# Kernel optimization log

Hardware: AMD Instinct MI355X
Metric: run time of the kernel (lower is better)

The kernel has to match this reference:

```python
import jax, jax.numpy as jnp
import numpy as np

HEADS = 8
GS = 16
C = 512
E = 512
SCALE = (E / HEADS) ** -0.5
PNAMES = ['sa_qkv_w','sa_qkv_b','sa_pa_w','sa_pa_b','sa_ln1_g','sa_ln1_b','sa_f1_w','sa_f1_b','sa_f2_w','sa_f2_b','sa_ln2_g','sa_ln2_b','sa_c1_w','sa_c1_b','sa_c2_w','sa_c2_b','sa_bn_g','sa_bn_b','ca_q_w','ca_q_b','ca_k_w','ca_k_b','ca_v_w','ca_v_b','ca_pa_w','ca_pa_b','p_q_w','p_q_b','p_k_w','p_k_b','p_v_w','p_v_b','p_pa_w','p_pa_b','p_ln_g','p_ln_b','p_lin_w','p_lin_b']


def _ln(x, g, b, eps=1e-5):
    m = x.mean(-1, keepdims=True)
    v = jnp.var(x, axis=-1, keepdims=True)
    return (x - m) / jnp.sqrt(v + eps) * g + b


def _conv1x1(x, w, b):
    return jnp.einsum('bchw,oc->bohw', x, w) + b[None, :, None, None]


def _up_ac(x, out=GS):
    # bilinear upsample, align_corners=True (nn.UpsamplingBilinear2d)
    H = x.shape[2]
    pos = jnp.arange(out) * (H - 1) / (out - 1)
    lo = jnp.floor(pos).astype(jnp.int32)
    hi = jnp.minimum(lo + 1, H - 1)
    w = (pos - lo).astype(x.dtype)
    xr = x[:, :, lo, :] * (1 - w)[None, None, :, None] + x[:, :, hi, :] * w[None, None, :, None]
    return xr[:, :, :, lo] * (1 - w) + xr[:, :, :, hi] * w


def _asri(x, p):
    # Sequence_ASRI: GAP tokens -> attention over the batch axis -> pixel-shuffle back
    B = x.shape[0]; ch = E // HEADS
    gap = x.mean((2, 3))                                             # [B,C]
    qkv = (gap @ p['sa_qkv_w'].T + p['sa_qkv_b']).reshape(B, 4, ch, HEADS).transpose(1, 3, 0, 2)  # [4,H,B,ch]
    q, k, v, skip = qkv[0], qkv[1], qkv[2], qkv[3]
    attn = jax.nn.softmax(jnp.einsum('hbc,hdc->hbd', q, k) * SCALE, -1)  # [H,B,B]
    o = jnp.einsum('hbd,hdc->hbc', attn, v)
    merge = lambda t: t.transpose(1, 2, 0).reshape(B, E)             # 'head b c -> b (c head)'
    a = merge(o) @ p['sa_pa_w'].T + p['sa_pa_b'] + merge(skip)
    h = jax.nn.relu(_ln(a, p['sa_ln1_g'], p['sa_ln1_b']) @ p['sa_f1_w'].T + p['sa_f1_b'])
    a = h @ p['sa_f2_w'].T + p['sa_f2_b'] + a
    s = _ln(a, p['sa_ln2_g'], p['sa_ln2_b']) @ p['sa_c1_w'].T + p['sa_c1_b']  # [B,C*16]
    s = _up_ac(s.reshape(B, C, 4, 4))                                 # pixel shuffle p1=p2=4 then bilinear to 16x16
    s = _conv1x1(s, p['sa_c2_w'], p['sa_c2_b'])
    # BatchNorm2d in eval mode (running_mean=0, running_var=1, eps=1e-5)
    s = s / np.float32(np.sqrt(1.0 + 1e-5)) * p['sa_bn_g'][None, :, None, None] + p['sa_bn_b'][None, :, None, None]
    return x + jax.nn.relu(s)


def _sscm(x1, x2, p):
    # Sequence_SSCM: GAP-token q/k over batch axis, full spatial v
    B = x1.shape[0]; ch = E // HEADS
    q = (x1.mean((2, 3)) @ p['ca_q_w'].T + p['ca_q_b']).reshape(B, ch, HEADS).transpose(2, 0, 1)  # [H,B,ch]
    k = (x2.mean((2, 3)) @ p['ca_k_w'].T + p['ca_k_b']).reshape(B, ch, HEADS).transpose(2, 0, 1)
    v = _conv1x1(x2, p['ca_v_w'], p['ca_v_b']).reshape(B, ch, HEADS, GS, GS).transpose(2, 0, 1, 3, 4).reshape(HEADS, B, ch * GS * GS)
    attn = jax.nn.softmax(jnp.einsum('hbc,hdc->hbd', q, k) * SCALE, -1)  # [H,B,B]
    o = jnp.einsum('hbd,hdm->hbm', attn, v)
    o = o.reshape(HEADS, B, ch, GS, GS).transpose(1, 2, 0, 3, 4).reshape(B, E, GS, GS)
    return jax.nn.relu(_conv1x1(o, p['ca_pa_w'], p['ca_pa_b']))


def _pixel(x1, x2, p):
    # Pixel_SSCM: pixel-wise cross-batch attention (no scale -- matches source)
    B = x1.shape[0]; ch = E // HEADS; N = GS * GS
    split = lambda t: t.reshape(B, ch, HEADS, N).transpose(2, 0, 3, 1)   # 'b (c head) h w -> head b (h w) c'
    q = split(_conv1x1(x1, p['p_q_w'], p['p_q_b']))                      # [H,B,N,ch]
    k = split(_conv1x1(x2, p['p_k_w'], p['p_k_b']))
    v = split(_conv1x1(x2, p['p_v_w'], p['p_v_b'])).reshape(HEADS, B * N, ch)
    attn = jax.nn.softmax(jnp.einsum('hbnc,hqmc->hbqnm', q, k), -1)      # [H,B,B,N,N]
    attn = attn.transpose(1, 0, 3, 2, 4).reshape(B, HEADS, N, B * N)     # 'head b q h w -> b head h (q w)'
    o = jnp.einsum('bhnm,hmc->bhnc', attn, v)
    o = o.transpose(0, 3, 1, 2).reshape(B, E, GS, GS)                    # 'b head (h w) c -> b (c head) h w'
    o = _conv1x1(o, p['p_pa_w'], p['p_pa_b']) + x1
    t = o.reshape(B, C, N).transpose(0, 2, 1)                            # [B,N,C]
    t = jax.nn.relu(_ln(t, p['p_ln_g'], p['p_ln_b']) @ p['p_lin_w'].T + p['p_lin_b'])
    return t.transpose(0, 2, 1).reshape(B, C, GS, GS)


def _hrlm(p, xs, xq):
    sa_s = _asri(xs, p)
    sa_q = _asri(xq, p)
    ca_s = _sscm(sa_s, sa_q, p)
    ca_q = _sscm(sa_q, sa_s, p)
    return _pixel(sa_s, ca_q, p), _pixel(sa_q, ca_s, p)


def setup_inputs():
    key = jax.random.key(0)
    ks = iter(jax.random.split(key, 64))
    w = lambda *s: (jax.random.normal(next(ks), s) * 0.02).astype(jnp.float32)
    z = lambda n: jnp.zeros((n,), jnp.float32)
    o = lambda n: jnp.ones((n,), jnp.float32)
    return dict(
        fea_support=jax.random.normal(next(ks), (8, C, GS, GS), jnp.float32),
        fea_query=jax.random.normal(next(ks), (8, C, GS, GS), jnp.float32),
        sa_qkv_w=w(4 * E, C), sa_qkv_b=z(4 * E),
        sa_pa_w=w(E, E), sa_pa_b=z(E),
        sa_ln1_g=o(E), sa_ln1_b=z(E),
        sa_f1_w=w(E, E), sa_f1_b=z(E), sa_f2_w=w(E, E), sa_f2_b=z(E),
        sa_ln2_g=o(E), sa_ln2_b=z(E),
        sa_c1_w=w(C * 16, E), sa_c1_b=z(C * 16),
        sa_c2_w=w(C, E), sa_c2_b=z(C),
        sa_bn_g=o(C), sa_bn_b=z(C),
        ca_q_w=w(E, C), ca_q_b=z(E), ca_k_w=w(E, C), ca_k_b=z(E),
        ca_v_w=w(E, C), ca_v_b=z(E), ca_pa_w=w(C, E), ca_pa_b=z(C),
        p_q_w=w(E, C), p_q_b=z(E), p_k_w=w(E, C), p_k_b=z(E),
        p_v_w=w(E, C), p_v_b=z(E), p_pa_w=w(C, E), p_pa_b=z(C),
        p_ln_g=o(C), p_ln_b=z(C), p_lin_w=w(C, C), p_lin_b=z(C),
    )


def reference(fea_support, fea_query, sa_qkv_w, sa_qkv_b, sa_pa_w, sa_pa_b, sa_ln1_g, sa_ln1_b, sa_f1_w, sa_f1_b, sa_f2_w, sa_f2_b, sa_ln2_g, sa_ln2_b, sa_c1_w, sa_c1_b, sa_c2_w, sa_c2_b, sa_bn_g, sa_bn_b, ca_q_w, ca_q_b, ca_k_w, ca_k_b, ca_v_w, ca_v_b, ca_pa_w, ca_pa_b, p_q_w, p_q_b, p_k_w, p_k_b, p_v_w, p_v_b, p_pa_w, p_pa_b, p_ln_g, p_ln_b, p_lin_w, p_lin_b):
    p = dict(zip(PNAMES, (sa_qkv_w, sa_qkv_b, sa_pa_w, sa_pa_b, sa_ln1_g, sa_ln1_b, sa_f1_w, sa_f1_b, sa_f2_w, sa_f2_b, sa_ln2_g, sa_ln2_b, sa_c1_w, sa_c1_b, sa_c2_w, sa_c2_b, sa_bn_g, sa_bn_b, ca_q_w, ca_q_b, ca_k_w, ca_k_b, ca_v_w, ca_v_b, ca_pa_w, ca_pa_b, p_q_w, p_q_b, p_k_w, p_k_b, p_v_w, p_v_b, p_pa_w, p_pa_b, p_ln_g, p_ln_b, p_lin_w, p_lin_b)))
    return _hrlm(p, fea_support, fea_query)
```

## Files before the change

### kernel.cpp

```cpp
#include <hip/hip_runtime.h>
#include <cmath>

#define IMG 131072
#define BIGF 1048576

#define CF_RELU  1
#define CF_RES   2
#define CF_BN    4
#define CF_SPLIT 8
#define CF_TRANS 16

typedef __attribute__((ext_vector_type(8))) short short8;
typedef __attribute__((ext_vector_type(4))) short short4v;
typedef __attribute__((ext_vector_type(4))) float f32x4;

__device__ __forceinline__ float wave_sum(float v){
    #pragma unroll
    for (int off = 32; off; off >>= 1) v += __shfl_xor(v, off);
    return v;
}

__device__ __forceinline__ unsigned short bf16_rn(float x){
    union { float f; unsigned u; } v; v.f = x;
    unsigned r = v.u + 0x7FFF + ((v.u >> 16) & 1);
    return (unsigned short)(r >> 16);
}
__device__ __forceinline__ float bf16_to_f(unsigned short h){
    union { float f; unsigned u; } v; v.u = ((unsigned)h) << 16;
    return v.f;
}
__device__ __forceinline__ unsigned pk_hi(unsigned a, unsigned b){
    return __builtin_amdgcn_perm(b, a, 0x05040100u);
}
__device__ __forceinline__ unsigned pk_lo(unsigned a, unsigned b){
    return __builtin_amdgcn_perm(b, a, 0x07060302u);
}

struct GapJobs  { const float* x[2]; float* o[2]; };
struct G8Job    { const float* in; const float* W; const float* bias; const float* add; float* out; };
struct G8Jobs   { G8Job j[4]; };
struct AAJobs   { const float* qkv[2]; float* om[2]; };
struct LnJobs   { const float* in[2]; float* out[2]; };
struct UpJobs   { const float* in[2]; float* out[2]; };
struct SAJobs   { const float* q8[2]; const float* k8[2]; float* aw[2]; };
struct SPJobs   { const float* aw[2]; const float* v[2]; float* out[2]; };
struct ZJobs    { float* p[2]; };
struct ConvJob  { const float* X; const float* W; const float* B; const float* R;
                  const float* bng; const float* bnb; float* O; int flags; };
struct ConvJobs { ConvJob j[6]; };
struct PixJob   { const unsigned* Q; const unsigned* K; const unsigned* V; float* O; };
struct PixJobs  { PixJob j[2]; };

__global__ __launch_bounds__(64) void k_gap(GapJobs jo){
    const int br = blockIdx.y;
    const int bc = blockIdx.x;
    const int lane = threadIdx.x;
    const float* p = jo.x[br] + (size_t)bc * 256;
    float s = p[lane] + p[lane + 64] + p[lane + 128] + p[lane + 192];
    s = wave_sum(s);
    if (lane == 0) jo.o[br][bc] = s * (1.0f / 256.0f);
}

__global__ __launch_bounds__(64) void k_gemm8(G8Jobs jo, int add_off, int add_stride, int O, int relu){
    const G8Job j = jo.j[blockIdx.y];
    const int o = blockIdx.x;
    const int lane = threadIdx.x;
    const float* wr = j.W + (size_t)o * 512;
    float acc[8] = {0,0,0,0,0,0,0,0};
    #pragma unroll
    for (int i = 0; i < 8; i++){
        float w = wr[lane + 64*i];
        #pragma unroll
        for (int b = 0; b < 8; b++) acc[b] += w * j.in[b*512 + lane + 64*i];
    }
    #pragma unroll
    for (int b = 0; b < 8; b++) acc[b] = wave_sum(acc[b]);
    if (lane < 8){
        float v = acc[0];
        #pragma unroll
        for (int b = 1; b < 8; b++) if (lane == b) v = acc[b];
        v += j.bias[o];
        if (j.add) v += j.add[lane*add_stride + add_off + o];
        if (relu) v = fmaxf(v, 0.f);
        j.out[(size_t)lane * O + o] = v;
    }
}

__global__ __launch_bounds__(64) void k_asri_attn(AAJobs jo){
    const int br = blockIdx.y;
    const float* qkv = jo.qkv[br];
    const int h = blockIdx.x >> 3, b = blockIdx.x & 7, c = threadIdx.x;
    const int ci = c*8 + h;
    float qc = qkv[b*2048 + ci];
    float s[8];
    #pragma unroll
    for (int d = 0; d < 8; d++){
        float p = qc * qkv[d*2048 + 512 + ci];
        p = wave_sum(p);
        s[d] = p * 0.125f;
    }
    float m = s[0];
    #pragma unroll
    for (int d = 1; d < 8; d++) m = fmaxf(m, s[d]);
    float sum = 0.f;
    #pragma unroll
    for (int d = 0; d < 8; d++){ s[d] = __expf(s[d]-m); sum += s[d]; }
    float r = 1.f / sum;
    float oc = 0.f;
    #pragma unroll
    for (int d = 0; d < 8; d++) oc += s[d]*r * qkv[d*2048 + 1024 + ci];
    jo.om[br][b*512 + ci] = oc;
}

__global__ __launch_bounds__(64) void k_ln8(LnJobs jo,
    const float* __restrict__ g, const float* __restrict__ be)
{
    const int br = blockIdx.y;
    const int b = blockIdx.x, lane = threadIdx.x;
    const float* in = jo.in[br];
    float v[8]; float s = 0.f;
    #pragma unroll
    for (int i = 0; i < 8; i++){ v[i] = in[b*512 + lane + 64*i]; s += v[i]; }
    s = wave_sum(s);
    float mean = s * (1.f/512.f);
    float q = 0.f;
    #pragma unroll
    for (int i = 0; i < 8; i++){ float d = v[i]-mean; q += d*d; }
    q = wave_sum(q);
    float rstd = rsqrtf(q*(1.f/512.f) + 1e-5f);
    #pragma unroll
    for (int i = 0; i < 8; i++){
        int c = lane + 64*i;
        jo.out[br][b*512 + c] = (v[i]-mean)*rstd*g[c] + be[c];
    }
}

__global__ __launch_bounds__(256) void k_up(UpJobs jo){
    const int br = blockIdx.y;
    const int idx = blockIdx.x*256 + threadIdx.x;
    const int x = idx & 15, y = (idx >> 4) & 15, bc = idx >> 8;
    float px = (float)(x*3) / 15.0f, py = (float)(y*3) / 15.0f;
    int lx = (int)px, ly = (int)py;
    float wx = px - lx, wy = py - ly;
    int hx = min(lx+1, 3), hy = min(ly+1, 3);
    const float* p = jo.in[br] + (size_t)bc * 16;
    float v00 = p[ly*4+lx], v01 = p[ly*4+hx], v10 = p[hy*4+lx], v11 = p[hy*4+hx];
    float a0 = v00*(1.f-wy) + v10*wy;
    float a1 = v01*(1.f-wy) + v11*wy;
    jo.out[br][idx] = a0*(1.f-wx) + a1*wx;
}

__global__ __launch_bounds__(256) void k_zero(ZJobs jo){
    jo.p[blockIdx.y][(size_t)blockIdx.x*256 + threadIdx.x] = 0.f;
}

#define LDK 40
__device__ __forceinline__ void convm_body(
    const float* __restrict__ Xb, const float* __restrict__ W,
    const float* __restrict__ bias, const float* __restrict__ resb,
    const float* __restrict__ bng, const float* __restrict__ bnb, float bninv,
    float* __restrict__ outb, int flags, int o0, int n0, unsigned short* lds)
{
    const int tid512 = threadIdx.x;
    const int g   = tid512 >> 8;
    const int tid = tid512 & 255;
    unsigned short* sAh = lds + g*10240;
    unsigned short* sAl = sAh + 2560;
    unsigned short* sBh = sAl + 2560;
    unsigned short* sBl = sBh + 2560;
    const int wv = tid >> 6, lane = tid & 63;
    const int quad = lane >> 4, l16 = lane & 15;
    const int wo = (wv >> 1) * 32, wn = (wv & 1) * 32;
    const int so  = tid >> 2, sk8 = (tid & 3) * 8;
    const int sp  = tid & 15, sn  = (tid >> 4) * 4;

    const bool trans = (flags & CF_TRANS) != 0;
    int so_g = o0 + so;
    if (trans) so_g = ((so_g & 63) << 3) | (so_g >> 6);

    const float* wrow = W + (size_t)so_g*512 + g*256 + sk8;
    const float* xrow = Xb + (size_t)(g*256 + 2*sp)*256 + n0 + sn;

    f32x4 acc[2][2] = {};
    float4 a0 = *(const float4*)(wrow);
    float4 a1 = *(const float4*)(wrow + 4);
    float4 x0 = *(const float4*)(xrow);
    float4 x1 = *(const float4*)(xrow + 256);

    for (int k0 = 0; k0 < 256; k0 += 32){
        __syncthreads();
        {
            float wa[8] = {a0.x,a0.y,a0.z,a0.w,a1.x,a1.y,a1.z,a1.w};
            #pragma unroll
            for (int j = 0; j < 4; j++){
                unsigned short h0 = bf16_rn(wa[2*j]);
                unsigned short h1 = bf16_rn(wa[2*j+1]);
                unsigned short g0 = bf16_rn(wa[2*j]   - bf16_to_f(h0));
                unsigned short g1 = bf16_rn(wa[2*j+1] - bf16_to_f(h1));
                *(unsigned*)&sAh[so*LDK + sk8 + 2*j] = (unsigned)h0 | ((unsigned)h1 << 16);
                *(unsigned*)&sAl[so*LDK + sk8 + 2*j] = (unsigned)g0 | ((unsigned)g1 << 16);
            }
            float xe[4] = {x0.x,x0.y,x0.z,x0.w};
            float xo[4] = {x1.x,x1.y,x1.z,x1.w};
            #pragma unroll
            for (int j = 0; j < 4; j++){
                unsigned short h0 = bf16_rn(xe[j]);
                unsigned short h1 = bf16_rn(xo[j]);
                unsigned short g0 = bf16_rn(xe[j] - bf16_to_f(h0));
                unsigned short g1 = bf16_rn(xo[j] - bf16_to_f(h1));
                *(unsigned*)&sBh[(sn+j)*LDK + 2*sp] = (unsigned)h0 | ((unsigned)h1 << 16);
                *(unsigned*)&sBl[(sn+j)*LDK + 2*sp] = (unsigned)g0 | ((unsigned)g1 << 16);
            }
        }
        __syncthreads();
        if (k0 + 32 < 256){
            a0 = *(const float4*)(wrow + k0 + 32);
            a1 = *(const float4*)(wrow + k0 + 36);
            x0 = *(const float4*)(xrow + (size_t)(k0+32)*256);
            x1 = *(const float4*)(xrow + (size_t)(k0+32)*256 + 256);
        }
        short8 ah[2], al[2], bh[2], bl[2];
        #pragma unroll
        for (int t = 0; t < 2; t++){
            int ai = (wo + 16*t + l16)*LDK + quad*8;
            ah[t] = *(const short8*)&sAh[ai];
            al[t] = *(const short8*)&sAl[ai];
            int bi = (wn + 16*t + l16)*LDK + quad*8;
            bh[t] = *(const short8*)&sBh[bi];
            bl[t] = *(const short8*)&sBl[bi];
        }
        if (trans){
            #pragma unroll
            for (int mt = 0; mt < 2; mt++){
                #pragma unroll
                for (int nt = 0; nt < 2; nt++){
                    acc[mt][nt] = __builtin_amdgcn_mfma_f32_16x16x32_bf16(bh[nt], ah[mt], acc[mt][nt], 0, 0, 0);
                    acc[mt][nt] = __builtin_amdgcn_mfma_f32_16x16x32_bf16(bl[nt], ah[mt], acc[mt][nt], 0, 0, 0);
                    acc[mt][nt] = __builtin_amdgcn_mfma_f32_16x16x32_bf16(bh[nt], al[mt], acc[mt][nt], 0, 0, 0);
                }
            }
        } else {
            #pragma unroll
            for (int mt = 0; mt < 2; mt++){
                #pragma unroll
                for (int nt = 0; nt < 2; nt++){
                    acc[mt][nt] = __builtin_amdgcn_mfma_f32_16x16x32_bf16(ah[mt], bh[nt], acc[mt][nt], 0, 0, 0);
                    acc[mt][nt] = __builtin_amdgcn_mfma_f32_16x16x32_bf16(ah[mt], bl[nt], acc[mt][nt], 0, 0, 0);
                    acc[mt][nt] = __builtin_amdgcn_mfma_f32_16x16x32_bf16(al[mt], bh[nt], acc[mt][nt], 0, 0, 0);
                }
            }
        }
    }
    __syncthreads();
    float* red = (float*)lds;
    if (g == 1){
        float* r = red + tid*20;
        #pragma unroll
        for (int mt = 0; mt < 2; mt++)
            #pragma unroll
            for (int nt = 0; nt < 2; nt++)
                *(f32x4*)(r + (mt*2+nt)*4) = acc[mt][nt];
    }
    __syncthreads();
    if (g == 0){
        float* r = red + tid*20;
        #pragma unroll
        for (int mt = 0; mt < 2; mt++)
            #pragma unroll
            for (int nt = 0; nt < 2; nt++){
                f32x4 o4 = *(const f32x4*)(r + (mt*2+nt)*4);
                acc[mt][nt] += o4;
            }
        if (trans){
            unsigned* op = (unsigned*)outb;
            #pragma unroll
            for (int mt = 0; mt < 2; mt++){
                #pragma unroll
                for (int nt = 0; nt < 2; nt++){
                    const int p  = o0 + wo + 16*mt + l16;
                    const int nb = n0 + wn + 16*nt + quad*4;
                    const int osrc = ((p & 63) << 3) | (p >> 6);
                    const float bs = bias[osrc];
                    #pragma unroll
                    for (int rr = 0; rr < 4; rr++){
                        float v = acc[mt][nt][rr] + bs;
                        unsigned short hi = bf16_rn(v);
                        unsigned short lo = bf16_rn(v - bf16_to_f(hi));
                        op[(size_t)(nb+rr)*512 + p] = (unsigned)hi | ((unsigned)lo << 16);
                    }
                }
            }
        } else {
            #pragma unroll
            for (int mt = 0; mt < 2; mt++){
                #pragma unroll
                for (int nt = 0; nt < 2; nt++){
                    const int n  = n0 + wn + 16*nt + l16;
                    const int ob = o0 + wo + 16*mt + quad*4;
                    #pragma unroll
                    for (int rr = 0; rr < 4; rr++){
                        const int o = ob + rr;
                        float v = acc[mt][nt][rr] + bias[o];
                        if (flags & CF_BN)   v = v*(bninv*bng[o]) + bnb[o];
                        if (flags & CF_RELU) v = fmaxf(v, 0.f);
                        if (flags & CF_RES)  v += resb[(size_t)o*256 + n];
                        if (flags & CF_SPLIT){
                            unsigned short hi = bf16_rn(v);
                            unsigned short lo = bf16_rn(v - bf16_to_f(hi));
                            unsigned pk = (unsigned)hi | ((unsigned)lo << 16);
                            ((unsigned*)outb)[(size_t)o*256 + n] = pk;
                        } else {
                            outb[(size_t)o*256 + n] = v;
                        }
                    }
                }
            }
        }
    }
}

__global__ __launch_bounds__(512) void k_convm(ConvJobs jo, float bninv)
{
    __shared__ unsigned short lds[20480];
    const int z = blockIdx.z;
    const ConvJob j = jo.j[z >> 3];
    const int b = z & 7;
    convm_body(j.X + (size_t)b*IMG, j.W, j.B, j.R ? j.R + (size_t)b*IMG : nullptr,
               j.bng, j.bnb, bninv, j.O + (size_t)b*IMG, j.flags,
               blockIdx.y*64, blockIdx.x*64, lds);
}

__global__ __launch_bounds__(64) void k_sscm_attn(SAJobs jo)
{
    const int br = blockIdx.y;
    const int h = blockIdx.x >> 3, b = blockIdx.x & 7, c = threadIdx.x;
    const int ci = c*8 + h;
    float qc = jo.q8[br][b*512 + ci];
    float s[8];
    #pragma unroll
    for (int d = 0; d < 8; d++){
        float p = qc * jo.k8[br][d*512 + ci];
        p = wave_sum(p);
        s[d] = p * 0.125f;
    }
    float m = s[0];
    #pragma unroll
    for (int d = 1; d < 8; d++) m = fmaxf(m, s[d]);
    float sum = 0.f;
    #pragma unroll
    for (int d = 0; d < 8; d++){ s[d] = __expf(s[d]-m); sum += s[d]; }
    float r = 1.f/sum;
    if (c < 8){
        float v = s[0];
        #pragma unroll
        for (int d = 1; d < 8; d++) if (c == d) v = s[d];
        jo.aw[br][blockIdx.x*8 + c] = v*r;
    }
}

__global__ __launch_bounds__(256) void k_sscm_apply(SPJobs jo)
{
    const int br = blockIdx.y;
    const int idx = blockIdx.x*256 + threadIdx.x;
    const int pix = idx & 255, e = (idx >> 8) & 511, b = idx >> 17;
    const int h = e & 7;
    const float* aw = jo.aw[br] + (h*8 + b)*8;
    const float* v = jo.v[br];
    float acc = 0.f;
    #pragma unroll
    for (int d = 0; d < 8; d++) acc += aw[d] * v[(size_t)d*IMG + (size_t)e*256 + pix];
    jo.out[br][idx] = acc;
}

__global__ __launch_bounds__(256) void k_pixel_mfma(PixJobs jo)
{
    __shared__ char smem[40960];
    unsigned short* sQh = (unsigned short*)smem;
    unsigned short* sQl = sQh + 2*64*40;
    unsigned short* sKh = sQl + 2*64*40;
    unsigned short* sKl = sKh + 2*64*40;
    unsigned short* sP  = (unsigned short*)smem;
    unsigned short* sVh = sKh;
    unsigned short* sVl = sKl;

    const int br = blockIdx.y >> 3, b = blockIdx.y & 7;
    const PixJob J = jo.j[br];
    const int nt = blockIdx.x & 3, d = blockIdx.x >> 2;
    const int h = blockIdx.z;
    const int tid = threadIdx.x;
    const int wv = tid >> 6, lane = tid & 63;
    const int quad = lane >> 4, l16 = lane & 15;
    const int n0 = nt * 64;

    {
        const unsigned* Qt = J.Q + (size_t)b*IMG + (size_t)n0*512 + h*64;
        const int q = tid >> 2, i0 = (tid & 3) * 16;
        const unsigned* src = Qt + (size_t)q*512 + i0;
        uint4 w0 = *(const uint4*)(src);
        uint4 w1 = *(const uint4*)(src + 4);
        uint4 w2 = *(const uint4*)(src + 8);
        uint4 w3 = *(const uint4*)(src + 12);
        unsigned hb[8], lb[8];
        hb[0]=pk_hi(w0.x,w0.y); hb[1]=pk_hi(w0.z,w0.w); hb[2]=pk_hi(w1.x,w1.y); hb[3]=pk_hi(w1.z,w1.w);
        hb[4]=pk_hi(w2.x,w2.y); hb[5]=pk_hi(w2.z,w2.w); hb[6]=pk_hi(w3.x,w3.y); hb[7]=pk_hi(w3.z,w3.w);
        lb[0]=pk_lo(w0.x,w0.y); lb[1]=pk_lo(w0.z,w0.w); lb[2]=pk_lo(w1.x,w1.y); lb[3]=pk_lo(w1.z,w1.w);
        lb[4]=pk_lo(w2.x,w2.y); lb[5]=pk_lo(w2.z,w2.w); lb[6]=pk_lo(w3.x,w3.y); lb[7]=pk_lo(w3.z,w3.w);
        int dst = (i0>>5)*2560 + q*40 + (i0&31);
        *(uint4*)&sQh[dst]     = *(uint4*)&hb[0];
        *(uint4*)&sQh[dst + 8] = *(uint4*)&hb[4];
        *(uint4*)&sQl[dst]     = *(uint4*)&lb[0];
        *(uint4*)&sQl[dst + 8] = *(uint4*)&lb[4];
    }
    __syncthreads();

    short8 bqh[2], bql[2];
    #pragma unroll
    for (int ks = 0; ks < 2; ks++){
        int idx = ks*2560 + (wv*16 + l16)*40 + quad*8;
        bqh[ks] = *(const short8*)&sQh[idx];
        bql[ks] = *(const short8*)&sQl[idx];
    }

    f32x4 S[16] = {};
    #pragma unroll
    for (int mq = 0; mq < 4; mq++){
        if (mq) __syncthreads();
        {
            const unsigned* Kt = J.K + (size_t)d*IMG + (size_t)(mq*64)*512 + h*64;
            const int mloc = tid & 63, cb0 = tid >> 6;
            #pragma unroll
            for (int p = 0; p < 2; p++){
                int cb = cb0 + 4*p;
                const unsigned* src = Kt + (size_t)mloc*512 + cb*8;
                uint4 wa = *(const uint4*)(src);
                uint4 wb = *(const uint4*)(src + 4);
                union { short8 s; unsigned u[4]; } hu, lu;
                hu.u[0]=pk_hi(wa.x,wa.y); hu.u[1]=pk_hi(wa.z,wa.w);
                hu.u[2]=pk_hi(wb.x,wb.y); hu.u[3]=pk_hi(wb.z,wb.w);
                lu.u[0]=pk_lo(wa.x,wa.y); lu.u[1]=pk_lo(wa.z,wa.w);
                lu.u[2]=pk_lo(wb.x,wb.y); lu.u[3]=pk_lo(wb.z,wb.w);
                int idx = (cb>>2)*2560 + mloc*40 + (cb&3)*8;
                *(short8*)&sKh[idx] = hu.s;
                *(short8*)&sKl[idx] = lu.s;
            }
        }
        __syncthreads();
        #pragma unroll
        for (int mtl = 0; mtl < 4; mtl++){
            int t = mq*4 + mtl;
            #pragma unroll
            for (int ks = 0; ks < 2; ks++){
                int idx = ks*2560 + (mtl*16 + l16)*40 + quad*8;
                short8 ah = *(const short8*)&sKh[idx];
                short8 al = *(const short8*)&sKl[idx];
                S[t] = __builtin_amdgcn_mfma_f32_16x16x32_bf16(ah, bqh[ks], S[t], 0, 0, 0);
                S[t] = __builtin_amdgcn_mfma_f32_16x16x32_bf16(ah, bql[ks], S[t], 0, 0, 0);
                S[t] = __builtin_amdgcn_mfma_f32_16x16x32_bf16(al, bqh[ks], S[t], 0, 0, 0);
            }
        }
    }

    {
        float mx = -3.4e38f;
        #pragma unroll
        for (int t = 0; t < 16; t++)
            #pragma unroll
            for (int r = 0; r < 4; r++) mx = fmaxf(mx, S[t][r]);
        mx = fmaxf(mx, __shfl_xor(mx, 16));
        mx = fmaxf(mx, __shfl_xor(mx, 32));
        float sum = 0.f;
        #pragma unroll
        for (int t = 0; t < 16; t++)
            #pragma unroll
            for (int r = 0; r < 4; r++){ S[t][r] = __expf(S[t][r]-mx); sum += S[t][r]; }
        sum += __shfl_xor(sum, 16);
        sum += __shfl_xor(sum, 32);
        float rr = 1.f/sum;
        #pragma unroll
        for (int t = 0; t < 16; t++)
            #pragma unroll
            for (int r = 0; r < 4; r++) S[t][r] *= rr;
    }

    f32x4 oac[4] = {};
    #pragma unroll
    for (int hm = 0; hm < 2; hm++){
        __syncthreads();
        #pragma unroll
        for (int mtl = 0; mtl < 8; mtl++){
            int t = hm*8 + mtl;
            short4v p4;
            #pragma unroll
            for (int r = 0; r < 4; r++) p4[r] = (short)bf16_rn(S[t][r]);
            int idx = (mtl>>1)*2560 + (wv*16 + l16)*40 + 16*(mtl&1) + quad*4;
            *(short4v*)&sP[idx] = p4;
        }
        #pragma unroll
        for (int sub = 0; sub < 2; sub++){
            if (sub) __syncthreads();
            {
                const unsigned* Vp = J.V + (size_t)d*IMG + (size_t)h*256 + hm*128 + sub*64;
                const int mp = tid & 31, c0 = tid >> 5;
                #pragma unroll
                for (int p = 0; p < 8; p++){
                    int c = c0 + 8*p;
                    const unsigned* src = Vp + (size_t)c*2048 + 2*mp;
                    uint2 w = *(const uint2*)(src);
                    int idx = ((2*mp)>>5)*2560 + c*40 + ((2*mp)&31);
                    *(unsigned*)&sVh[idx] = pk_hi(w.x, w.y);
                    *(unsigned*)&sVl[idx] = pk_lo(w.x, w.y);
                }
            }
            __syncthreads();
            #pragma unroll
            for (int l = 0; l < 2; l++){
                int gks = sub*2 + l;
                int pidx = gks*2560 + (wv*16 + l16)*40 + quad*8;
                short8 bp = *(const short8*)&sP[pidx];
                #pragma unroll
                for (int ct = 0; ct < 4; ct++){
                    int vidx = l*2560 + (ct*16 + l16)*40 + quad*8;
                    short8 vh = *(const short8*)&sVh[vidx];
                    short8 vl = *(const short8*)&sVl[vidx];
                    oac[ct] = __builtin_amdgcn_mfma_f32_16x16x32_bf16(vh, bp, oac[ct], 0, 0, 0);
                    oac[ct] = __builtin_amdgcn_mfma_f32_16x16x32_bf16(vl, bp, oac[ct], 0, 0, 0);
                }
            }
        }
    }

    {
        float* Ob = J.O + (size_t)b * IMG;
        const int q = n0 + wv*16 + l16;
        #pragma unroll
        for (int ct = 0; ct < 4; ct++){
            #pragma unroll
            for (int r = 0; r < 4; r++){
                int c = ct*16 + quad*4 + r;
                unsafeAtomicAdd(&Ob[(size_t)(c*8+h)*256 + q], oac[ct][r]);
            }
        }
    }
}

__global__ __launch_bounds__(64) void k_ln_pix(LnJobs jo,
    const float* __restrict__ g, const float* __restrict__ be)
{
    const int br = blockIdx.y;
    const int bn = blockIdx.x;
    const int b = bn >> 8, n = bn & 255;
    const int lane = threadIdx.x;
    const float* p = jo.in[br] + (size_t)b*IMG + n;
    float v[8]; float s = 0.f;
    #pragma unroll
    for (int i = 0; i < 8; i++){ v[i] = p[(size_t)(lane + 64*i)*256]; s += v[i]; }
    s = wave_sum(s);
    float mean = s * (1.f/512.f);
    float q = 0.f;
    #pragma unroll
    for (int i = 0; i < 8; i++){ float d = v[i]-mean; q += d*d; }
    q = wave_sum(q);
    float rstd = rsqrtf(q*(1.f/512.f) + 1e-5f);
    #pragma unroll
    for (int i = 0; i < 8; i++){
        int c = lane + 64*i;
        jo.out[br][(size_t)b*IMG + (size_t)c*256 + n] = (v[i]-mean)*rstd*g[c] + be[c];
    }
}

extern "C" void kernel_launch(void* const* d_in, const int* in_sizes, int n_in,
                              void* d_out, int out_size, void* d_ws, size_t ws_size,
                              hipStream_t stream)
{
    const float* xs    = (const float*)d_in[0];
    const float* xq    = (const float*)d_in[1];
    const float* qkvw  = (const float*)d_in[2];  const float* qkvb = (const float*)d_in[3];
    const float* paw   = (const float*)d_in[4];  const float* pab  = (const float*)d_in[5];
    const float* ln1g  = (const float*)d_in[6];  const float* ln1b = (const float*)d_in[7];
    const float* f1w   = (const float*)d_in[8];  const float* f1b  = (const float*)d_in[9];
    const float* f2w   = (const float*)d_in[10]; const float* f2b  = (const float*)d_in[11];
    const float* ln2g  = (const float*)d_in[12]; const float* ln2b = (const float*)d_in[13];
    const float* c1w   = (const float*)d_in[14]; const float* c1b  = (const float*)d_in[15];
    const float* c2w   = (const float*)d_in[16]; const float* c2b  = (const float*)d_in[17];
    const float* bng   = (const float*)d_in[18]; const float* bnb  = (const float*)d_in[19];
    const float* caqw  = (const float*)d_in[20]; const float* caqb = (const float*)d_in[21];
    const float* cakw  = (const float*)d_in[22]; const float* cakb = (const float*)d_in[23];
    const float* cavw  = (const float*)d_in[24]; const float* cavb = (const float*)d_in[25];
    const float* capw  = (const float*)d_in[26]; const float* capb = (const float*)d_in[27];
    const float* pqw   = (const float*)d_in[28]; const float* pqb  = (const float*)d_in[29];
    const float* pkw   = (const float*)d_in[30]; const float* pkb  = (const float*)d_in[31];
    const float* pvw   = (const float*)d_in[32]; const float* pvb  = (const float*)d_in[33];
    const float* ppw   = (const float*)d_in[34]; const float* ppb  = (const float*)d_in[35];
    const float* plng  = (const float*)d_in[36]; const float* plnb = (const float*)d_in[37];
    const float* plinw = (const float*)d_in[38]; const float* plinb= (const float*)d_in[39];

    const size_t SMF = 262144;
    float* ws = (float*)d_ws;
    float* smb = ws;
    float* B[12];
    for (int i = 0; i < 12; i++) B[i] = ws + SMF + (size_t)i*BIGF;
    float* sa_s = B[0]; float* sa_q = B[1];
    float* ca_s = B[2]; float* ca_q = B[3];
    const bool paired_pixel = ws_size >= (SMF + 12*(size_t)BIGF)*sizeof(float) + 1024;

    auto SM = [&](int br){ return smb + (size_t)br*131072; };
    auto GAP=[&](int br){ return SM(br); };            auto QKV=[&](int br){ return SM(br)+4096; };
    auto OM =[&](int br){ return SM(br)+20480; };      auto AA =[&](int br){ return SM(br)+24576; };
    auto HB =[&](int br){ return SM(br)+28672; };      auto A2 =[&](int br){ return SM(br)+32768; };
    auto LNB=[&](int br){ return SM(br)+36864; };      auto S8 =[&](int br){ return SM(br)+40960; };
    auto ATW=[&](int br){ return SM(br)+106496; };     auto Q8 =[&](int br){ return SM(br)+107008; };
    auto K8 =[&](int br){ return SM(br)+111104; };

    const float bninv = 1.0f / sqrtf(1.0f + 1e-5f);
    float* out0 = (float*)d_out;
    float* out1 = out0 + (size_t)BIGF;

    {
        GapJobs gj = {{xs, xq}, {GAP(0), GAP(1)}};
        k_gap<<<dim3(4096,2), 64, 0, stream>>>(gj);
        G8Jobs qj = {{{GAP(0), qkvw, qkvb, nullptr, QKV(0)}, {GAP(1), qkvw, qkvb, nullptr, QKV(1)}}};
        k_gemm8<<<dim3(2048,2), 64, 0, stream>>>(qj, 0, 0, 2048, 0);
        AAJobs aj = {{QKV(0), QKV(1)}, {OM(0), OM(1)}};
        k_asri_attn<<<dim3(64,2), 64, 0, stream>>>(aj);
        G8Jobs pj = {{{OM(0), paw, pab, QKV(0), AA(0)}, {OM(1), paw, pab, QKV(1), AA(1)}}};
        k_gemm8<<<dim3(512,2), 64, 0, stream>>>(pj, 1536, 2048, 512, 0);
        LnJobs l1 = {{AA(0), AA(1)}, {LNB(0), LNB(1)}};
        k_ln8<<<dim3(8,2), 64, 0, stream>>>(l1, ln1g, ln1b);
        G8Jobs fj = {{{LNB(0), f1w, f1b, nullptr, HB(0)}, {LNB(1), f1w, f1b, nullptr, HB(1)}}};
        k_gemm8<<<dim3(512,2), 64, 0, stream>>>(fj, 0, 0, 512, 1);
        G8Jobs f2j = {{{HB(0), f2w, f2b, AA(0), A2(0)}, {HB(1), f2w, f2b, AA(1), A2(1)}}};
        k_gemm8<<<dim3(512,2), 64, 0, stream>>>(f2j, 0, 512, 512, 0);
        LnJobs l2 = {{A2(0), A2(1)}, {LNB(0), LNB(1)}};
        k_ln8<<<dim3(8,2), 64, 0, stream>>>(l2, ln2g, ln2b);
        G8Jobs cj = {{{LNB(0), c1w, c1b, nullptr, S8(0)}, {LNB(1), c1w, c1b, nullptr, S8(1)}}};
        k_gemm8<<<dim3(8192,2), 64, 0, stream>>>(cj, 0, 0, 8192, 0);
        UpJobs uj = {{S8(0), S8(1)}, {B[4], B[5]}};
        k_up<<<dim3(4096,2), 256, 0, stream>>>(uj);
        ConvJobs c2j = {};
        c2j.j[0] = {B[4], c2w, c2b, xs, bng, bnb, sa_s, CF_BN|CF_RELU|CF_RES};
        c2j.j[1] = {B[5], c2w, c2b, xq, bng, bnb, sa_q, CF_BN|CF_RELU|CF_RES};
        k_convm<<<dim3(4,8,16), 512, 0, stream>>>(c2j, bninv);
    }

    {
        GapJobs gj = {{sa_s, sa_q}, {GAP(0), GAP(1)}};
        k_gap<<<dim3(4096,2), 64, 0, stream>>>(gj);
        G8Jobs qj = {{{GAP(0), caqw, caqb, nullptr, Q8(0)},
                      {GAP(1), cakw, cakb, nullptr, K8(0)},
                      {GAP(1), caqw, caqb, nullptr, Q8(1)},
                      {GAP(0), cakw, cakb, nullptr, K8(1)}}};
        k_gemm8<<<dim3(512,4), 64, 0, stream>>>(qj, 0, 0, 512, 0);
        SAJobs sj = {{Q8(0), Q8(1)}, {K8(0), K8(1)}, {ATW(0), ATW(1)}};
        k_sscm_attn<<<dim3(64,2), 64, 0, stream>>>(sj);
        ConvJobs vj = {};
        vj.j[0] = {sa_q, cavw, cavb, nullptr, nullptr, nullptr, B[4], 0};
        vj.j[1] = {sa_s, cavw, cavb, nullptr, nullptr, nullptr, B[5], 0};
        k_convm<<<dim3(4,8,16), 512, 0, stream>>>(vj, 1.f);
        SPJobs pj = {{ATW(0), ATW(1)}, {B[4], B[5]}, {B[6], B[7]}};
        k_sscm_apply<<<dim3(4096,2), 256, 0, stream>>>(pj);
        ConvJobs aj = {};
        aj.j[0] = {B[6], capw, capb, nullptr, nullptr, nullptr, ca_s, CF_RELU};
        aj.j[1] = {B[7], capw, capb, nullptr, nullptr, nullptr, ca_q, CF_RELU};
        k_convm<<<dim3(4,8,16), 512, 0, stream>>>(aj, 1.f);
    }

    if (paired_pixel){
        ConvJobs qkvj = {};
        qkvj.j[0] = {sa_s, pqw, pqb, nullptr, nullptr, nullptr, B[4],  CF_SPLIT|CF_TRANS};
        qkvj.j[1] = {ca_q, pkw, pkb, nullptr, nullptr, nullptr, B[5],  CF_SPLIT|CF_TRANS};
        qkvj.j[2] = {ca_q, pvw, pvb, nullptr, nullptr, nullptr, B[6],  CF_SPLIT};
        qkvj.j[3] = {sa_q, pqw, pqb, nullptr, nullptr, nullptr, B[8],  CF_SPLIT|CF_TRANS};
        qkvj.j[4] = {ca_s, pkw, pkb, nullptr, nullptr, nullptr, B[9],  CF_SPLIT|CF_TRANS};
        qkvj.j[5] = {ca_s, pvw, pvb, nullptr, nullptr, nullptr, B[10], CF_SPLIT};
        k_convm<<<dim3(4,8,48), 512, 0, stream>>>(qkvj, 1.f);
        ZJobs zj = {{B[7], B[11]}};
        k_zero<<<dim3(4096,2), 256, 0, stream>>>(zj);
        PixJobs pxj = {{{(const unsigned*)B[4], (const unsigned*)B[5], (const unsigned*)B[6], B[7]},
                        {(const unsigned*)B[8], (const unsigned*)B[9], (const unsigned*)B[10], B[11]}}};
        k_pixel_mfma<<<dim3(32,16,8), 256, 0, stream>>>(pxj);
        ConvJobs ppj = {};
        ppj.j[0] = {B[7],  ppw, ppb, sa_s, nullptr, nullptr, out0, CF_RES};
        ppj.j[1] = {B[11], ppw, ppb, sa_q, nullptr, nullptr, out1, CF_RES};
        k_convm<<<dim3(4,8,16), 512, 0, stream>>>(ppj, 1.f);
        LnJobs lj = {{out0, out1}, {B[4], B[8]}};
        k_ln_pix<<<dim3(2048,2), 64, 0, stream>>>(lj, plng, plnb);
        ConvJobs lnj = {};
        lnj.j[0] = {B[4], plinw, plinb, nullptr, nullptr, nullptr, out0, CF_RELU};
        lnj.j[1] = {B[8], plinw, plinb, nullptr, nullptr, nullptr, out1, CF_RELU};
        k_convm<<<dim3(4,8,16), 512, 0, stream>>>(lnj, 1.f);
    } else {
        auto pixel1 = [&](const float* x1, const float* x2, float* out){
            ConvJobs qkvj = {};
            qkvj.j[0] = {x1, pqw, pqb, nullptr, nullptr, nullptr, B[4], CF_SPLIT|CF_TRANS};
            qkvj.j[1] = {x2, pkw, pkb, nullptr, nullptr, nullptr, B[5], CF_SPLIT|CF_TRANS};
            qkvj.j[2] = {x2, pvw, pvb, nullptr, nullptr, nullptr, B[6], CF_SPLIT};
            k_convm<<<dim3(4,8,24), 512, 0, stream>>>(qkvj, 1.f);
            ZJobs zj = {{B[7], B[7]}};
            k_zero<<<dim3(4096,1), 256, 0, stream>>>(zj);
            PixJobs pxj = {{{(const unsigned*)B[4], (const unsigned*)B[5], (const unsigned*)B[6], B[7]},
                            {(const unsigned*)B[4], (const unsigned*)B[5], (const unsigned*)B[6], B[7]}}};
            k_pixel_mfma<<<dim3(32,8,8), 256, 0, stream>>>(pxj);
            ConvJobs ppj = {};
            ppj.j[0] = {B[7], ppw, ppb, x1, nullptr, nullptr, out, CF_RES};
            k_convm<<<dim3(4,8,8), 512, 0, stream>>>(ppj, 1.f);
            LnJobs lj = {{out, out}, {B[4], B[4]}};
            k_ln_pix<<<dim3(2048,1), 64, 0, stream>>>(lj, plng, plnb);
            ConvJobs lnj = {};
            lnj.j[0] = {B[4], plinw, plinb, nullptr, nullptr, nullptr, out, CF_RELU};
            k_convm<<<dim3(4,8,8), 512, 0, stream>>>(lnj, 1.f);
        };
        pixel1(sa_s, ca_q, out0);
        pixel1(sa_q, ca_s, out1);
    }

    (void)in_sizes; (void)n_in; (void)out_size;
}
```

Baseline: 473.6 us.

## Pre-split weights and activations into packed bf16 hi/lo once for reuse

A new kernel converts the eight conv weight matrices into packed bf16 hi/lo pairs once per call. Selected conv outputs also write a packed split copy that later convs load directly, so they skip the per-tile bf16 split arithmetic in the LDS staging loop. This removes repeated conversion ALU work across the many blocks that reuse the same weights and activations. In exchange it adds an extra weight pass, extra output writes, and workspace use. The new paths are gated on workspace size.

```diff
diff --git a/kernel.cpp b/kernel.cpp
--- a/kernel.cpp
+++ b/kernel.cpp
@@ -28,6 +28,11 @@
 __device__ __forceinline__ float bf16_to_f(unsigned short h){
     union { float f; unsigned u; } v; v.u = ((unsigned)h) << 16;
     return v.f;
+}
+__device__ __forceinline__ unsigned pack_split(float x){
+    unsigned short hi = bf16_rn(x);
+    unsigned short lo = bf16_rn(x - bf16_to_f(hi));
+    return (unsigned)hi | ((unsigned)lo << 16);
 }
 __device__ __forceinline__ unsigned pk_hi(unsigned a, unsigned b){
     return __builtin_amdgcn_perm(b, a, 0x05040100u);
@@ -45,8 +50,10 @@
 struct SAJobs   { const float* q8[2]; const float* k8[2]; float* aw[2]; };
 struct SPJobs   { const float* aw[2]; const float* v[2]; float* out[2]; };
 struct ZJobs    { float* p[2]; };
+struct WsJobs   { const float* w[8]; unsigned* o; };
 struct ConvJob  { const float* X; const float* W; const float* B; const float* R;
-                  const float* bng; const float* bnb; float* O; int flags; };
+                  const float* bng; const float* bnb; float* O; int flags;
+                  const unsigned* Wpk; const unsigned* Xpk; unsigned* O2; };
 struct ConvJobs { ConvJob j[6]; };
 struct PixJob   { const unsigned* Q; const unsigned* K; const unsigned* V; float* O; };
 struct PixJobs  { PixJob j[2]; };
@@ -154,12 +161,24 @@
     jo.p[blockIdx.y][(size_t)blockIdx.x*256 + threadIdx.x] = 0.f;
 }
 
+__global__ __launch_bounds__(256) void k_wsplit(WsJobs jo){
+    const int m = blockIdx.y;
+    const int i = (blockIdx.x*256 + threadIdx.x)*4;
+    float4 v = *(const float4*)(jo.w[m] + i);
+    uint4 r;
+    r.x = pack_split(v.x); r.y = pack_split(v.y);
+    r.z = pack_split(v.z); r.w = pack_split(v.w);
+    *(uint4*)(jo.o + (size_t)m*262144 + i) = r;
+}
+
 #define LDK 40
 __device__ __forceinline__ void convm_body(
-    const float* __restrict__ Xb, const float* __restrict__ W,
+    const float* __restrict__ Xb, const unsigned* __restrict__ Xpk,
+    const float* __restrict__ W,  const unsigned* __restrict__ Wpk,
     const float* __restrict__ bias, const float* __restrict__ resb,
     const float* __restrict__ bng, const float* __restrict__ bnb, float bninv,
-    float* __restrict__ outb, int flags, int o0, int n0, unsigned short* lds)
+    float* __restrict__ outb, unsigned* __restrict__ o2b,
+    int flags, int o0, int n0, unsigned short* lds)
 {
     const int tid512 = threadIdx.x;
     const int g   = tid512 >> 8;
@@ -178,18 +197,30 @@
     int so_g = o0 + so;
     if (trans) so_g = ((so_g & 63) << 3) | (so_g >> 6);
 
-    const float* wrow = W + (size_t)so_g*512 + g*256 + sk8;
-    const float* xrow = Xb + (size_t)(g*256 + 2*sp)*256 + n0 + sn;
+    const float*    wrow  = W + (size_t)so_g*512 + g*256 + sk8;
+    const unsigned* wprow = Wpk ? Wpk + (size_t)so_g*512 + g*256 + sk8 : nullptr;
+    const float*    xrow  = Xb + (size_t)(g*256 + 2*sp)*256 + n0 + sn;
+    const unsigned* xprow = Xpk ? Xpk + (size_t)(g*256 + 2*sp)*256 + n0 + sn : nullptr;
 
     f32x4 acc[2][2] = {};
-    float4 a0 = *(const float4*)(wrow);
-    float4 a1 = *(const float4*)(wrow + 4);
-    float4 x0 = *(const float4*)(xrow);
-    float4 x1 = *(const float4*)(xrow + 256);
+    float4 a0, a1, x0, x1;
+    uint4 pw0, pw1, px0, px1;
+    if (Wpk){ pw0 = *(const uint4*)(wprow); pw1 = *(const uint4*)(wprow + 4); }
+    else    { a0  = *(const float4*)(wrow); a1  = *(const float4*)(wrow + 4); }
+    if (Xpk){ px0 = *(const uint4*)(xprow); px1 = *(const uint4*)(xprow + 256); }
+    else    { x0  = *(const float4*)(xrow); x1  = *(const float4*)(xrow + 256); }
 
     for (int k0 = 0; k0 < 256; k0 += 32){
         __syncthreads();
-        {
+        if (Wpk){
+            uint4 h4, l4;
+            h4.x = pk_hi(pw0.x, pw0.y); h4.y = pk_hi(pw0.z, pw0.w);
+            h4.z = pk_hi(pw1.x, pw1.y); h4.w = pk_hi(pw1.z, pw1.w);
+            l4.x = pk_lo(pw0.x, pw0.y); l4.y = pk_lo(pw0.z, pw0.w);
+            l4.z = pk_lo(pw1.x, pw1.y); l4.w = pk_lo(pw1.z, pw1.w);
+            *(uint4*)&sAh[so*LDK + sk8] = h4;
+            *(uint4*)&sAl[so*LDK + sk8] = l4;
+        } else {
             float wa[8] = {a0.x,a0.y,a0.z,a0.w,a1.x,a1.y,a1.z,a1.w};
             #pragma unroll
             for (int j = 0; j < 4; j++){
@@ -200,6 +231,17 @@
                 *(unsigned*)&sAh[so*LDK + sk8 + 2*j] = (unsigned)h0 | ((unsigned)h1 << 16);
                 *(unsigned*)&sAl[so*LDK + sk8 + 2*j] = (unsigned)g0 | ((unsigned)g1 << 16);
             }
+        }
+        if (Xpk){
+            *(unsigned*)&sBh[(sn+0)*LDK + 2*sp] = pk_hi(px0.x, px1.x);
+            *(unsigned*)&sBl[(sn+0)*LDK + 2*sp] = pk_lo(px0.x, px1.x);
+            *(unsigned*)&sBh[(sn+1)*LDK + 2*sp] = pk_hi(px0.y, px1.y);
+            *(unsigned*)&sBl[(sn+1)*LDK + 2*sp] = pk_lo(px0.y, px1.y);
+            *(unsigned*)&sBh[(sn+2)*LDK + 2*sp] = pk_hi(px0.z, px1.z);
+            *(unsigned*)&sBl[(sn+2)*LDK + 2*sp] = pk_lo(px0.z, px1.z);
+            *(unsigned*)&sBh[(sn+3)*LDK + 2*sp] = pk_hi(px0.w, px1.w);
+            *(unsigned*)&sBl[(sn+3)*LDK + 2*sp] = pk_lo(px0.w, px1.w);
+        } else {
             float xe[4] = {x0.x,x0.y,x0.z,x0.w};
             float xo[4] = {x1.x,x1.y,x1.z,x1.w};
             #pragma unroll
@@ -214,10 +256,10 @@
         }
         __syncthreads();
         if (k0 + 32 < 256){
-            a0 = *(const float4*)(wrow + k0 + 32);
-            a1 = *(const float4*)(wrow + k0 + 36);
-            x0 = *(const float4*)(xrow + (size_t)(k0+32)*256);
-            x1 = *(const float4*)(xrow + (size_t)(k0+32)*256 + 256);
+            if (Wpk){ pw0 = *(const uint4*)(wprow + k0 + 32); pw1 = *(const uint4*)(wprow + k0 + 36); }
+            else    { a0  = *(const float4*)(wrow + k0 + 32); a1  = *(const float4*)(wrow + k0 + 36); }
+            if (Xpk){ px0 = *(const uint4*)(xprow + (size_t)(k0+32)*256); px1 = *(const uint4*)(xprow + (size_t)(k0+32)*256 + 256); }
+            else    { x0  = *(const float4*)(xrow + (size_t)(k0+32)*256); x1  = *(const float4*)(xrow + (size_t)(k0+32)*256 + 256); }
         }
         short8 ah[2], al[2], bh[2], bl[2];
         #pragma unroll
@@ -284,9 +326,7 @@
                     #pragma unroll
                     for (int rr = 0; rr < 4; rr++){
                         float v = acc[mt][nt][rr] + bs;
-                        unsigned short hi = bf16_rn(v);
-                        unsigned short lo = bf16_rn(v - bf16_to_f(hi));
-                        op[(size_t)(nb+rr)*512 + p] = (unsigned)hi | ((unsigned)lo << 16);
+                        op[(size_t)(nb+rr)*512 + p] = pack_split(v);
                     }
                 }
             }
@@ -305,12 +345,10 @@
                         if (flags & CF_RELU) v = fmaxf(v, 0.f);
                         if (flags & CF_RES)  v += resb[(size_t)o*256 + n];
                         if (flags & CF_SPLIT){
-                            unsigned short hi = bf16_rn(v);
-                            unsigned short lo = bf16_rn(v - bf16_to_f(hi));
-                            unsigned pk = (unsigned)hi | ((unsigned)lo << 16);
-                            ((unsigned*)outb)[(size_t)o*256 + n] = pk;
+                            ((unsigned*)outb)[(size_t)o*256 + n] = pack_split(v);
                         } else {
                             outb[(size_t)o*256 + n] = v;
+                            if (o2b) o2b[(size_t)o*256 + n] = pack_split(v);
                         }
                     }
                 }
@@ -325,9 +363,14 @@
     const int z = blockIdx.z;
     const ConvJob j = jo.j[z >> 3];
     const int b = z & 7;
-    convm_body(j.X + (size_t)b*IMG, j.W, j.B, j.R ? j.R + (size_t)b*IMG : nullptr,
-               j.bng, j.bnb, bninv, j.O + (size_t)b*IMG, j.flags,
-               blockIdx.y*64, blockIdx.x*64, lds);
+    convm_body(j.X + (size_t)b*IMG,
+               j.Xpk ? j.Xpk + (size_t)b*IMG : nullptr,
+               j.W, j.Wpk, j.B,
+               j.R ? j.R + (size_t)b*IMG : nullptr,
+               j.bng, j.bnb, bninv,
+               j.O + (size_t)b*IMG,
+               j.O2 ? j.O2 + (size_t)b*IMG : nullptr,
+               j.flags, blockIdx.y*64, blockIdx.x*64, lds);
 }
 
 __global__ __launch_bounds__(64) void k_sscm_attn(SAJobs jo)
@@ -602,6 +645,13 @@
     float* sa_s = B[0]; float* sa_q = B[1];
     float* ca_s = B[2]; float* ca_q = B[3];
     const bool paired_pixel = ws_size >= (SMF + 12*(size_t)BIGF)*sizeof(float) + 1024;
+    const bool has_wpk = ws_size >= (SMF + 14*(size_t)BIGF)*sizeof(float) + 1024;
+    const bool has_xpk = ws_size >= (SMF + 18*(size_t)BIGF)*sizeof(float) + 1024;
+    unsigned* WPK = has_wpk ? (unsigned*)(ws + SMF + 12*(size_t)BIGF) : nullptr;
+    unsigned* XP[4] = {nullptr, nullptr, nullptr, nullptr};
+    if (has_xpk)
+        for (int i = 0; i < 4; i++) XP[i] = (unsigned*)(ws + SMF + (size_t)(14+i)*BIGF);
+    auto wp = [&](int m){ return WPK ? (const unsigned*)(WPK + (size_t)m*262144) : (const unsigned*)nullptr; };
 
     auto SM = [&](int br){ return smb + (size_t)br*131072; };
     auto GAP=[&](int br){ return SM(br); };            auto QKV=[&](int br){ return SM(br)+4096; };
@@ -614,6 +664,11 @@
     const float bninv = 1.0f / sqrtf(1.0f + 1e-5f);
     float* out0 = (float*)d_out;
     float* out1 = out0 + (size_t)BIGF;
+
+    if (WPK){
+        WsJobs wj = {{c2w, cavw, capw, pqw, pkw, pvw, ppw, plinw}, WPK};
+        k_wsplit<<<dim3(256,8), 256, 0, stream>>>(wj);
+    }
 
     {
         GapJobs gj = {{xs, xq}, {GAP(0), GAP(1)}};
@@ -637,8 +692,8 @@
         UpJobs uj = {{S8(0), S8(1)}, {B[4], B[5]}};
         k_up<<<dim3(4096,2), 256, 0, stream>>>(uj);
         ConvJobs c2j = {};
-        c2j.j[0] = {B[4], c2w, c2b, xs, bng, bnb, sa_s, CF_BN|CF_RELU|CF_RES};
-        c2j.j[1] = {B[5], c2w, c2b, xq, bng, bnb, sa_q, CF_BN|CF_RELU|CF_RES};
+        c2j.j[0] = {B[4], c2w, c2b, xs, bng, bnb, sa_s, CF_BN|CF_RELU|CF_RES, wp(0), nullptr, XP[0]};
+        c2j.j[1] = {B[5], c2w, c2b, xq, bng, bnb, sa_q, CF_BN|CF_RELU|CF_RES, wp(0), nullptr, XP[1]};
         k_convm<<<dim3(4,8,16), 512, 0, stream>>>(c2j, bninv);
     }
 
@@ -653,25 +708,25 @@
         SAJobs sj = {{Q8(0), Q8(1)}, {K8(0), K8(1)}, {ATW(0), ATW(1)}};
         k_sscm_attn<<<dim3(64,2), 64, 0, stream>>>(sj);
         ConvJobs vj = {};
-        vj.j[0] = {sa_q, cavw, cavb, nullptr, nullptr, nullptr, B[4], 0};
-        vj.j[1] = {sa_s, cavw, cavb, nullptr, nullptr, nullptr, B[5], 0};
+        vj.j[0] = {sa_q, cavw, cavb, nullptr, nullptr, nullptr, B[4], 0, wp(1), XP[1], nullptr};
+        vj.j[1] = {sa_s, cavw, cavb, nullptr, nullptr, nullptr, B[5], 0, wp(1), XP[0], nullptr};
         k_convm<<<dim3(4,8,16), 512, 0, stream>>>(vj, 1.f);
         SPJobs pj = {{ATW(0), ATW(1)}, {B[4], B[5]}, {B[6], B[7]}};
         k_sscm_apply<<<dim3(4096,2), 256, 0, stream>>>(pj);
         ConvJobs aj = {};
-        aj.j[0] = {B[6], capw, capb, nullptr, nullptr, nullptr, ca_s, CF_RELU};
-        aj.j[1] = {B[7], capw, capb, nullptr, nullptr, nullptr, ca_q, CF_RELU};
+        aj.j[0] = {B[6], capw, capb, nullptr, nullptr, nullptr, ca_s, CF_RELU, wp(2), nullptr, XP[2]};
+        aj.j[1] = {B[7], capw, capb, nullptr, nullptr, nullptr, ca_q, CF_RELU, wp(2), nullptr, XP[3]};
         k_convm<<<dim3(4,8,16), 512, 0, stream>>>(aj, 1.f);
     }
 
     if (paired_pixel){
         ConvJobs qkvj = {};
-        qkvj.j[0] = {sa_s, pqw, pqb, nullptr, nullptr, nullptr, B[4],  CF_SPLIT|CF_TRANS};
-        qkvj.j[1] = {ca_q, pkw, pkb, nullptr, nullptr, nullptr, B[5],  CF_SPLIT|CF_TRANS};
-        qkvj.j[2] = {ca_q, pvw, pvb, nullptr, nullptr, nullptr, B[6],  CF_SPLIT};
-        qkvj.j[3] = {sa_q, pqw, pqb, nullptr, nullptr, nullptr, B[8],  CF_SPLIT|CF_TRANS};
-        qkvj.j[4] = {ca_s, pkw, pkb, nullptr, nullptr, nullptr, B[9],  CF_SPLIT|CF_TRANS};
-        qkvj.j[5] = {ca_s, pvw, pvb, nullptr, nullptr, nullptr, B[10], CF_SPLIT};
+        qkvj.j[0] = {sa_s, pqw, pqb, nullptr, nullptr, nullptr, B[4],  CF_SPLIT|CF_TRANS, wp(3), XP[0], nullptr};
+        qkvj.j[1] = {ca_q, pkw, pkb, nullptr, nullptr, nullptr, B[5],  CF_SPLIT|CF_TRANS, wp(4), XP[3], nullptr};
+        qkvj.j[2] = {ca_q, pvw, pvb, nullptr, nullptr, nullptr, B[6],  CF_SPLIT,          wp(5), XP[3], nullptr};
+        qkvj.j[3] = {sa_q, pqw, pqb, nullptr, nullptr, nullptr, B[8],  CF_SPLIT|CF_TRANS, wp(3), XP[1], nullptr};
+        qkvj.j[4] = {ca_s, pkw, pkb, nullptr, nullptr, nullptr, B[9],  CF_SPLIT|CF_TRANS, wp(4), XP[2], nullptr};
+        qkvj.j[5] = {ca_s, pvw, pvb, nullptr, nullptr, nullptr, B[10], CF_SPLIT,          wp(5), XP[2], nullptr};
         k_convm<<<dim3(4,8,48), 512, 0, stream>>>(qkvj, 1.f);
         ZJobs zj = {{B[7], B[11]}};
         k_zero<<<dim3(4096,2), 256, 0, stream>>>(zj);
@@ -679,21 +734,21 @@
                         {(const unsigned*)B[8], (const unsigned*)B[9], (const unsigned*)B[10], B[11]}}};
         k_pixel_mfma<<<dim3(32,16,8), 256, 0, stream>>>(pxj);
         ConvJobs ppj = {};
-        ppj.j[0] = {B[7],  ppw, ppb, sa_s, nullptr, nullptr, out0, CF_RES};
-        ppj.j[1] = {B[11], ppw, ppb, sa_q, nullptr, nullptr, out1, CF_RES};
+        ppj.j[0] = {B[7],  ppw, ppb, sa_s, nullptr, nullptr, out0, CF_RES, wp(6), nullptr, nullptr};
+        ppj.j[1] = {B[11], ppw, ppb, sa_q, nullptr, nullptr, out1, CF_RES, wp(6), nullptr, nullptr};
         k_convm<<<dim3(4,8,16), 512, 0, stream>>>(ppj, 1.f);
         LnJobs lj = {{out0, out1}, {B[4], B[8]}};
         k_ln_pix<<<dim3(2048,2), 64, 0, stream>>>(lj, plng, plnb);
         ConvJobs lnj = {};
-        lnj.j[0] = {B[4], plinw, plinb, nullptr, nullptr, nullptr, out0, CF_RELU};
-        lnj.j[1] = {B[8], plinw, plinb, nullptr, nullptr, nullptr, out1, CF_RELU};
+        lnj.j[0] = {B[4], plinw, plinb, nullptr, nullptr, nullptr, out0, CF_RELU, wp(7), nullptr, nullptr};
+        lnj.j[1] = {B[8], plinw, plinb, nullptr, nullptr, nullptr, out1, CF_RELU, wp(7), nullptr, nullptr};
         k_convm<<<dim3(4,8,16), 512, 0, stream>>>(lnj, 1.f);
     } else {
         auto pixel1 = [&](const float* x1, const float* x2, float* out){
             ConvJobs qkvj = {};
-            qkvj.j[0] = {x1, pqw, pqb, nullptr, nullptr, nullptr, B[4], CF_SPLIT|CF_TRANS};
-            qkvj.j[1] = {x2, pkw, pkb, nullptr, nullptr, nullptr, B[5], CF_SPLIT|CF_TRANS};
-            qkvj.j[2] = {x2, pvw, pvb, nullptr, nullptr, nullptr, B[6], CF_SPLIT};
+            qkvj.j[0] = {x1, pqw, pqb, nullptr, nullptr, nullptr, B[4], CF_SPLIT|CF_TRANS, wp(3), nullptr, nullptr};
+            qkvj.j[1] = {x2, pkw, pkb, nullptr, nullptr, nullptr, B[5], CF_SPLIT|CF_TRANS, wp(4), nullptr, nullptr};
+            qkvj.j[2] = {x2, pvw, pvb, nullptr, nullptr, nullptr, B[6], CF_SPLIT,          wp(5), nullptr, nullptr};
             k_convm<<<dim3(4,8,24), 512, 0, stream>>>(qkvj, 1.f);
             ZJobs zj = {{B[7], B[7]}};
             k_zero<<<dim3(4096,1), 256, 0, stream>>>(zj);
@@ -701,12 +756,12 @@
                             {(const unsigned*)B[4], (const unsigned*)B[5], (const unsigned*)B[6], B[7]}}};
             k_pixel_mfma<<<dim3(32,8,8), 256, 0, stream>>>(pxj);
             ConvJobs ppj = {};
-            ppj.j[0] = {B[7], ppw, ppb, x1, nullptr, nullptr, out, CF_RES};
+            ppj.j[0] = {B[7], ppw, ppb, x1, nullptr, nullptr, out, CF_RES, wp(6), nullptr, nullptr};
             k_convm<<<dim3(4,8,8), 512, 0, stream>>>(ppj, 1.f);
             LnJobs lj = {{out, out}, {B[4], B[4]}};
             k_ln_pix<<<dim3(2048,1), 64, 0, stream>>>(lj, plng, plnb);
             ConvJobs lnj = {};
-            lnj.j[0] = {B[4], plinw, plinb, nullptr, nullptr, nullptr, out, CF_RELU};
+            lnj.j[0] = {B[4], plinw, plinb, nullptr, nullptr, nullptr, out, CF_RELU, wp(7), nullptr, nullptr};
             k_convm<<<dim3(4,8,8), 512, 0, stream>>>(lnj, 1.f);
         };
         pixel1(sa_s, ca_q, out0);
```

After: 489.3 us. 3.3% more time.
